# Performance work log

Measured on AMD Instinct MI355X. Metric: run time of the kernel, lower is better.

Reference implementation:

```python
import jax, jax.numpy as jnp
import numpy as np

B, D, H, O, E, R, K, NH = 2048, 512, 2048, 512, 8, 4, 2, 8
DH = O // NH
EPS = 1e-5

def _ln(x, g, b):
    m = x.mean(-1, keepdims=True)
    v = ((x - m) ** 2).mean(-1, keepdims=True)
    return (x - m) / jnp.sqrt(v + EPS) * g + b

def setup_inputs():
    key = jax.random.key(0)
    ks = jax.random.split(key, 16)
    n = lambda k, shape, fan: jax.random.normal(k, shape, jnp.float32) * (fan ** -0.5)
    x = jax.random.normal(ks[0], (B, D), jnp.float32)
    regime = jax.random.randint(ks[1], (B,), 0, R)
    regime_features = jax.nn.one_hot(regime, R, dtype=jnp.float32)
    return dict(
        x=x, regime=regime, regime_features=regime_features,
        ew1=n(ks[2], (R, E, D, H), D), eb1=jnp.zeros((R, E, H)),
        lng=jnp.ones((R, E, H)), lnb=jnp.zeros((R, E, H)),
        ew2=n(ks[3], (R, E, H, O), H), eb2=jnp.zeros((R, E, O)),
        rw1=n(ks[4], (R, D + R, H), D + R), rb1=jnp.zeros((R, H)),
        rw2=n(ks[5], (R, H, E), H), rb2=jnp.zeros((R, E)),
        ipw=n(ks[6], (3 * O, O), O), ipb=jnp.zeros((3 * O,)),
        opw=n(ks[7], (O, O), O), opb=jnp.zeros((O,)),
        ang=jnp.ones((O,)), anb=jnp.zeros((O,)),
    )

def _forward(x, regime, regime_features, ew1, eb1, lng, lnb, ew2, eb2, rw1, rb1, rw2, rb2, ipw, ipb, opw, opb, ang, anb):
    B_ = x.shape[0]
    bi = jnp.arange(B_)
    # regime-conditioned routing: compute logits for all regimes densely, select per sample
    ri = jnp.concatenate([x, regime_features], axis=-1)                  # [B, D+R]
    rh = jax.nn.relu(jnp.einsum('bf,rfh->rbh', ri, rw1) + rb1[:, None])
    logits = (jnp.einsum('rbh,rhe->rbe', rh, rw2) + rb2[:, None])[regime, bi]  # [B, E]
    w = jax.nn.softmax(logits, axis=-1)
    tkw, tki = jax.lax.top_k(w, K)
    tkw = tkw / tkw.sum(-1, keepdims=True)
    # experts: all regimes x all experts, then select the per-sample regime block
    h = jnp.einsum('bd,redh->rebh', x, ew1) + eb1[:, :, None]            # [R, E, B, H]
    h = jax.nn.relu(_ln(h, lng[:, :, None], lnb[:, :, None]))
    eo = jnp.einsum('rebh,reho->rebo', h, ew2) + eb2[:, :, None] + x[None, None]  # identity residual (D == O)
    eo = eo.transpose(0, 2, 1, 3)[regime, bi]                            # [B, E, O]
    # group attention over expert axis (torch MultiheadAttention, eval mode)
    qkv = eo @ ipw.T + ipb
    q, k, v = jnp.split(qkv, 3, axis=-1)
    sh = lambda t: t.reshape(B_, E, NH, DH).transpose(0, 2, 1, 3)
    q, k, v = sh(q), sh(k), sh(v)
    attn = jax.nn.softmax(jnp.einsum('bhqd,bhkd->bhqk', q, k) / np.sqrt(DH).astype(np.float32), axis=-1)
    av = jnp.einsum('bhqk,bhkd->bhqd', attn, v).transpose(0, 2, 1, 3).reshape(B_, E, O)
    eo = _ln(eo + av @ opw.T + opb, ang, anb)
    # top-k combine
    gathered = jnp.take_along_axis(eo, tki[:, :, None], axis=1)          # [B, K, O]
    return jnp.sum(tkw[:, :, None] * gathered, axis=1)

def reference(x, regime, regime_features, ew1, eb1, lng, lnb, ew2, eb2, rw1, rb1, rw2, rb2, ipw, ipb, opw, opb, ang, anb):
    return _forward(x, regime, regime_features, ew1, eb1, lng, lnb, ew2, eb2, rw1, rb1, rw2, rb2, ipw, ipb, opw, opb, ang, anb)
```

## Files before the change

### kernel.cpp

```cpp
#include <hip/hip_runtime.h>
#include <hip/hip_bf16.h>
#include <cstddef>

typedef __attribute__((ext_vector_type(8))) short short8;
typedef __attribute__((ext_vector_type(4))) float f32x4;

constexpr int CB = 2048;
constexpr int CD = 512;
constexpr int CH = 2048;
constexpr int CO = 512;
constexpr int CE = 8;
constexpr int CR = 4;
constexpr int MBY = 5;

__device__ __forceinline__ float bs2f(short s){
  union { float f; unsigned u; } u; u.u = ((unsigned)(unsigned short)s) << 16; return u.f;
}
__device__ __forceinline__ short f2bs(float x){
  union { __hip_bfloat16 h; short s; } u; u.h = __float2bfloat16(x); return u.s;
}

#define GLL(g, l) __builtin_amdgcn_global_load_lds((const __attribute__((address_space(1))) void*)(g), (__attribute__((address_space(3))) void*)(l), 16, 0, 0)

__device__ __forceinline__ short8 ln8(short8 raw, float mean, float rstd,
                                      float4 g01, float4 g23, float4 b01, float4 b23){
  const float g[8] = {g01.x,g01.y,g01.z,g01.w,g23.x,g23.y,g23.z,g23.w};
  const float b[8] = {b01.x,b01.y,b01.z,b01.w,b23.x,b23.y,b23.z,b23.w};
  short8 o;
#pragma unroll
  for (int j = 0; j < 8; j++){
    const float v = (bs2f(raw[j]) - mean) * rstd * g[j] + b[j];
    o[j] = f2bs(fmaxf(v, 0.f));
  }
  return o;
}

__device__ __forceinline__ void block_reduce2(float& a, float& b){
#pragma unroll
  for (int off = 32; off; off >>= 1){ a += __shfl_xor(a, off, 64); b += __shfl_xor(b, off, 64); }
  __shared__ float sa[4], sb[4];
  const int wid = threadIdx.x >> 6, lane = threadIdx.x & 63;
  __syncthreads();
  if (lane == 0){ sa[wid] = a; sb[wid] = b; }
  __syncthreads();
  a = sa[0] + sa[1] + sa[2] + sa[3];
  b = sb[0] + sb[1] + sb[2] + sb[3];
}

__global__ __launch_bounds__(1024) void k_bucket(const int* __restrict__ regime,
                                                 int* __restrict__ meta, int* __restrict__ perm){
  __shared__ int cnt[4], cur[4];
  const int t = threadIdx.x;
  if (t < 4) cnt[t] = 0;
  __syncthreads();
  const int r0 = regime[t];
  const int r1 = regime[t + 1024];
  atomicAdd(&cnt[r0], 1);
  atomicAdd(&cnt[r1], 1);
  __syncthreads();
  if (t == 0){
    const int c0 = cnt[0], c1 = cnt[1], c2 = cnt[2], c3 = cnt[3];
    meta[0] = 0; meta[1] = c0; meta[2] = c0 + c1; meta[3] = c0 + c1 + c2; meta[4] = c0 + c1 + c2 + c3;
    cur[0] = 0; cur[1] = c0; cur[2] = c0 + c1; cur[3] = c0 + c1 + c2;
  }
  __syncthreads();
  { int p = atomicAdd(&cur[r0], 1); perm[p] = t; }
  { int p = atomicAdd(&cur[r1], 1); perm[p] = t + 1024; }
}

__device__ __forceinline__ void cvtt_tile(float (*tile)[65], const float* __restrict__ in,
                                          short* __restrict__ outp, int K, int N,
                                          int bx, int by, int bz){
  const int k0 = by * 64, n0 = bx * 64;
  const float* src = in + (size_t)bz * K * N;
  short* dst = outp + (size_t)bz * K * N;
  const int t = threadIdx.x;
  const int kk = t >> 4, nq = (t & 15) * 4;
#pragma unroll
  for (int j = 0; j < 4; j++){
    float4 v = *(const float4*)(src + (size_t)(k0 + kk + j * 16) * N + n0 + nq);
    tile[kk + j * 16][nq] = v.x; tile[kk + j * 16][nq + 1] = v.y;
    tile[kk + j * 16][nq + 2] = v.z; tile[kk + j * 16][nq + 3] = v.w;
  }
  __syncthreads();
  const int n = t >> 2, kq = (t & 3) * 16;
  short8 o0, o1;
#pragma unroll
  for (int j = 0; j < 8; j++) o0[j] = f2bs(tile[kq + j][n]);
#pragma unroll
  for (int j = 0; j < 8; j++) o1[j] = f2bs(tile[kq + 8 + j][n]);
  short* drow = dst + (size_t)(n0 + n) * K + k0 + kq;
  *(short8*)(drow) = o0;
  *(short8*)(drow + 8) = o1;
}

__global__ __launch_bounds__(256) void k_prep(
    const float* __restrict__ x, const int* __restrict__ perm,
    short* __restrict__ xp, short* __restrict__ xd,
    const float* __restrict__ rw1, const float* __restrict__ rb1,
    short* __restrict__ wtR, float* __restrict__ rbias,
    const float* __restrict__ ew1, short* __restrict__ wt1){
  __shared__ float tile[64][65];
  const int s = blockIdx.x;
  const int t = threadIdx.x;
  if (s < 2048){
    const int i = s, b = perm[i], c = t * 2;
    float2 v = *(const float2*)(x + (size_t)b * CD + c);
    short2 hi; hi.x = f2bs(v.x); hi.y = f2bs(v.y);
    short2 lo; lo.x = f2bs(v.x - bs2f(hi.x)); lo.y = f2bs(v.y - bs2f(hi.y));
    *(short2*)(xp + (size_t)i * CD + c) = hi;
    short* row = xd + (size_t)i * 1536;
    *(short2*)(row + c) = hi;
    *(short2*)(row + 512 + c) = hi;
    *(short2*)(row + 1024 + c) = lo;
    return;
  }
  if (s < 3072){
    const int i = s - 2048;
    const int bx = i & 31, by = (i >> 5) & 7, r = i >> 8;
    const int k0 = by * 64, n0 = bx * 64;
    const float* src = rw1 + (size_t)r * (CD + CR) * CH;
    short* dst = wtR + (size_t)r * CH * 1536;
    if (by == 0 && t < 64){
      const int n = n0 + t;
      rbias[r * CH + n] = rb1[(size_t)r * CH + n] + src[((size_t)(CD + r)) * CH + n];
    }
    const int kk = t >> 4, nq = (t & 15) * 4;
#pragma unroll
    for (int j = 0; j < 4; j++){
      float4 v = *(const float4*)(src + (size_t)(k0 + kk + j * 16) * CH + n0 + nq);
      tile[kk + j * 16][nq] = v.x; tile[kk + j * 16][nq + 1] = v.y;
      tile[kk + j * 16][nq + 2] = v.z; tile[kk + j * 16][nq + 3] = v.w;
    }
    __syncthreads();
    const int n = t >> 2, kq = (t & 3) * 16;
    short8 h0, h1, l0, l1;
#pragma unroll
    for (int j = 0; j < 8; j++){
      float f = tile[kq + j][n];
      short h = f2bs(f); h0[j] = h; l0[j] = f2bs(f - bs2f(h));
    }
#pragma unroll
    for (int j = 0; j < 8; j++){
      float f = tile[kq + 8 + j][n];
      short h = f2bs(f); h1[j] = h; l1[j] = f2bs(f - bs2f(h));
    }
    short* drow = dst + (size_t)(n0 + n) * 1536;
    *(short8*)(drow + k0 + kq) = h0;        *(short8*)(drow + k0 + kq + 8) = h1;
    *(short8*)(drow + 512 + k0 + kq) = l0;  *(short8*)(drow + 512 + k0 + kq + 8) = l1;
    *(short8*)(drow + 1024 + k0 + kq) = h0; *(short8*)(drow + 1024 + k0 + kq + 8) = h1;
    return;
  }
  {
    const int i = s - 3072;
    cvtt_tile(tile, ew1, wt1, CD, CH, i & 31, (i >> 5) & 7, i >> 8);
  }
}

__device__ __forceinline__ void logits_body(int blk,
    const float* __restrict__ part, const float* __restrict__ rb2,
    const int* __restrict__ meta, const int* __restrict__ perm,
    int* __restrict__ tki, float* __restrict__ tkw, int* __restrict__ qrows){
  const int wid = threadIdx.x >> 6, lane = threadIdx.x & 63;
  const int i = blk * 4 + wid;
  const int r = (i >= meta[1]) + (i >= meta[2]) + (i >= meta[3]);
  const int p0 = lane >> 3, e = lane & 7;
  float v = 0.f;
#pragma unroll
  for (int j = 0; j < 4; j++)
    v += part[((size_t)(p0 + 8 * j) * CB + i) * 8 + e];
  v += __shfl_xor(v, 8, 64);
  v += __shfl_xor(v, 16, 64);
  v += __shfl_xor(v, 32, 64);
  v += rb2[r * CE + e];
  float l8[8];
#pragma unroll
  for (int e2 = 0; e2 < 8; e2++) l8[e2] = __shfl(v, e2, 64);
  if (lane == 0){
    int i1 = 0; float m1 = l8[0];
#pragma unroll
    for (int e2 = 1; e2 < 8; e2++) if (l8[e2] > m1){ m1 = l8[e2]; i1 = e2; }
    int i2 = -1; float m2 = -1e30f;
#pragma unroll
    for (int e2 = 0; e2 < 8; e2++) if (e2 != i1 && l8[e2] > m2){ m2 = l8[e2]; i2 = e2; }
    const float e2w = __expf(m2 - m1);
    const float w1 = 1.f / (1.f + e2w);
    const int b = perm[i];
    tki[b * 2] = i1; tki[b * 2 + 1] = i2;
    tkw[b * 2] = w1; tkw[b * 2 + 1] = e2w * w1;
    qrows[b * 2] = b * CE + i1; qrows[b * 2 + 1] = b * CE + i2;
  }
}

template<int EPI, int NB>
__device__ __forceinline__ void gemm_body(
    short* __restrict__ ldsb,
    int bx, int by, int bz,
    const short* __restrict__ A, long lda,
    const short* __restrict__ Wt, long ldw,
    const int* __restrict__ goff, int fixedM, int Ksub, int N,
    const float* __restrict__ bias, long bstride,
    short* __restrict__ outb, float* __restrict__ outf,
    const int* __restrict__ operm, const float* __restrict__ xtra,
    float* __restrict__ pstat){
  constexpr int BK = 32;
  constexpr int BSTR = 4096 + NB * 1024;

  const int z = bz;
  int g0 = 0, Mg = fixedM;
  if (goff){ const int r = (EPI == 6) ? z : (z >> 3); g0 = goff[r]; Mg = goff[r + 1] - g0; }
  const int m0 = by * 128;
  if (m0 >= Mg) return;
  const int n0 = bx * (NB * 32);
  const int e = z & 7;

  const short* Ab;
  if constexpr (EPI == 1 || EPI == 6) Ab = A + (size_t)g0 * (size_t)lda;
  else Ab = A;
  const short* Wb = Wt + (size_t)z * (size_t)N * (size_t)ldw;

  const int tid = threadIdx.x;
  const int lane = tid & 63, wid = tid >> 6;
  const int srow = lane >> 2;
  const int sc = (((lane & 3) ^ ((srow >> 1) & 3)) << 3);

  int ar0 = m0 + wid * 32 + srow;
  int ar1 = ar0 + 16;
  if (ar0 > Mg - 1) ar0 = Mg - 1;
  if (ar1 > Mg - 1) ar1 = Mg - 1;
  if constexpr (EPI == 3){
    if (operm){ ar0 = operm[ar0]; ar1 = operm[ar1]; }
  }
  const short* ga0 = Ab + (size_t)ar0 * lda + sc;
  const short* ga1 = Ab + (size_t)ar1 * lda + sc;
  const int brow = n0 + wid * (NB * 8) + srow;
  const short* gb0 = Wb + (size_t)brow * ldw + sc;
  const short* gb1 = gb0 + (size_t)16 * ldw;

  const int wm = (wid >> 1) * 64, wn = (wid & 1) * (NB * 16);
  const int r16 = lane & 15, kb = lane >> 4;
  const int rsw = (r16 >> 1) & 3;

  f32x4 acc[4][NB];
#pragma unroll
  for (int a = 0; a < 4; a++)
#pragma unroll
    for (int b = 0; b < NB; b++) acc[a][b] = (f32x4){0.f, 0.f, 0.f, 0.f};

  const int NT = Ksub / BK;
  int buf = 0;

  {
    short* dA = ldsb + wid * 1024;
    short* dB = ldsb + 4096 + wid * (NB * 256);
    GLL(ga0, dA); GLL(ga1, dA + 512);
    GLL(gb0, dB);
    if constexpr (NB == 4){ GLL(gb1, dB + 512); }
  }
  __syncthreads();

  for (int t = 0; t < NT; ++t){
    if (t + 1 < NT){
      const int kof = (t + 1) * BK;
      short* dA = ldsb + (buf ^ 1) * BSTR + wid * 1024;
      short* dB = ldsb + (buf ^ 1) * BSTR + 4096 + wid * (NB * 256);
      GLL(ga0 + kof, dA); GLL(ga1 + kof, dA + 512);
      GLL(gb0 + kof, dB);
      if constexpr (NB == 4){ GLL(gb1 + kof, dB + 512); }
    }
    const short* sA = ldsb + buf * BSTR;
    const short* sB = sA + 4096;
    short8 af[4], bfv[NB];
#pragma unroll
    for (int mi = 0; mi < 4; mi++)
      af[mi] = *(const short8*)(sA + (wm + mi * 16 + r16) * 32 + ((kb ^ rsw) << 3));
#pragma unroll
    for (int ni = 0; ni < NB; ni++)
      bfv[ni] = *(const short8*)(sB + (wn + ni * 16 + r16) * 32 + ((kb ^ rsw) << 3));
#pragma unroll
    for (int mi = 0; mi < 4; mi++)
#pragma unroll
      for (int ni = 0; ni < NB; ni++)
        acc[mi][ni] = __builtin_amdgcn_mfma_f32_16x16x32_bf16(af[mi], bfv[ni], acc[mi][ni], 0, 0, 0);
    __syncthreads();
    buf ^= 1;
  }

  if constexpr (EPI == 1){
    const int slot = bx * 2 + (wid & 1);
#pragma unroll
    for (int mi = 0; mi < 4; mi++){
#pragma unroll
      for (int q = 0; q < 4; q++){
        const int i = m0 + wm + mi * 16 + kb * 4 + q;
        float vv[NB]; float sv = 0.f, sq = 0.f;
#pragma unroll
        for (int ni = 0; ni < NB; ni++){
          const int n = n0 + wn + ni * 16 + r16;
          const float v = acc[mi][ni][q] + bias[(size_t)z * bstride + n];
          vv[ni] = v; sv += v; sq += v * v;
        }
#pragma unroll
        for (int off = 1; off < 16; off <<= 1){
          sv += __shfl_xor(sv, off, 64);
          sq += __shfl_xor(sq, off, 64);
        }
        if (i < Mg){
#pragma unroll
          for (int ni = 0; ni < NB; ni++){
            const int n = n0 + wn + ni * 16 + r16;
            outb[((size_t)e * CB + (g0 + i)) * (size_t)N + n] = f2bs(vv[ni]);
          }
          if (r16 == 0){
            float* sp = pstat + ((size_t)slot * (CE * CB) + (size_t)e * CB + (g0 + i)) * 2;
            sp[0] = sv; sp[1] = sq;
          }
        }
      }
    }
    return;
  }

  if constexpr (EPI == 6){
    const int hbase = n0 + wn;
    float wv[NB][8]; float rbv[NB];
#pragma unroll
    for (int ni = 0; ni < NB; ni++){
      const int h = hbase + ni * 16 + r16;
      rbv[ni] = bias[(size_t)z * CH + h];
      const float* wp = xtra + ((size_t)z * CH + h) * 8;
#pragma unroll
      for (int e2 = 0; e2 < 8; e2++) wv[ni][e2] = wp[e2];
    }
    const int slot = bx * 2 + (wid & 1);
#pragma unroll
    for (int mi = 0; mi < 4; mi++){
#pragma unroll
      for (int q = 0; q < 4; q++){
        float tmp[8];
#pragma unroll
        for (int e2 = 0; e2 < 8; e2++) tmp[e2] = 0.f;
#pragma unroll
        for (int ni = 0; ni < NB; ni++){
          const float v = fmaxf(acc[mi][ni][q] + rbv[ni], 0.f);
#pragma unroll
          for (int e2 = 0; e2 < 8; e2++) tmp[e2] += v * wv[ni][e2];
        }
#pragma unroll
        for (int e2 = 0; e2 < 8; e2++){
          tmp[e2] += __shfl_xor(tmp[e2], 1, 64);
          tmp[e2] += __shfl_xor(tmp[e2], 2, 64);
          tmp[e2] += __shfl_xor(tmp[e2], 4, 64);
          tmp[e2] += __shfl_xor(tmp[e2], 8, 64);
        }
        const int row = wm + mi * 16 + kb * 4 + q;
        if (r16 == 0 && m0 + row < Mg){
          float* dp = outf + ((size_t)slot * CB + (g0 + m0 + row)) * 8;
#pragma unroll
          for (int e2 = 0; e2 < 8; e2++) dp[e2] = tmp[e2];
        }
      }
    }
    return;
  }

#pragma unroll
  for (int mi = 0; mi < 4; mi++){
#pragma unroll
    for (int q = 0; q < 4; q++){
      const int i = m0 + wm + mi * 16 + kb * 4 + q;
      if (i >= Mg) continue;
#pragma unroll
      for (int ni = 0; ni < NB; ni++){
        const int n = n0 + wn + ni * 16 + r16;
        float v = acc[mi][ni][q] + bias[n];
        if constexpr (EPI == 3){
          outb[(size_t)i * (size_t)N + n] = f2bs(v);
        } else {
          outf[(size_t)i * (size_t)N + n] = v;
        }
      }
    }
  }
}

__global__ __launch_bounds__(256) void k_rg1(
    const short* __restrict__ xp, const short* __restrict__ wt1, const int* __restrict__ meta,
    const float* __restrict__ eb1, short* __restrict__ hact, float* __restrict__ pstat,
    const short* __restrict__ xd, const short* __restrict__ wtR,
    const float* __restrict__ rbias, const float* __restrict__ rw2, float* __restrict__ part,
    const float* __restrict__ ew2, short* __restrict__ wt2,
    const float* __restrict__ ipw, short* __restrict__ ipwb,
    const float* __restrict__ opw, short* __restrict__ opwb){
  __shared__ __align__(16) short lds[2][8192];
  const int s = blockIdx.x;
  if (s < 320){
    const int bx = s & 15, by = (s >> 4) % MBY, bz = s / (16 * MBY);
    gemm_body<6, 4>(&lds[0][0], bx, by, bz, xd, 1536, wtR, 1536, meta, 0, 1536, CH,
                    rbias, 0, nullptr, part, nullptr, rw2, nullptr);
  } else if (s < 2880){
    const int t = s - 320;
    const int l = (t & 7) * 320 + (t >> 3);
    const int bx = l % 16; const int u = l / 16; const int by = u % MBY; const int bz = u / MBY;
    gemm_body<1, 4>(&lds[0][0], bx, by, bz, xp, CD, wt1, CD, meta, 0, CD, CH, eb1, CH,
                    hact, nullptr, nullptr, nullptr, pstat);
  } else if (s < 11072){
    float (*tile)[65] = (float(*)[65])&lds[0][0];
    const int i = s - 2880;
    cvtt_tile(tile, ew2, wt2, CH, CO, i & 7, (i >> 3) & 31, i >> 8);
  } else {
    int i = ((s - 11072) * 256 + threadIdx.x) * 8;
    const int na = 1536 * 512, nb = 512 * 512;
    const float* src; short* dst;
    if (i < na){ src = ipw + i; dst = ipwb + i; }
    else { int j = i - na; if (j >= nb) return; src = opw + j; dst = opwb + j; }
    float4 u = *(const float4*)(src);
    float4 v = *(const float4*)(src + 4);
    short8 o;
    o[0]=f2bs(u.x); o[1]=f2bs(u.y); o[2]=f2bs(u.z); o[3]=f2bs(u.w);
    o[4]=f2bs(v.x); o[5]=f2bs(v.y); o[6]=f2bs(v.z); o[7]=f2bs(v.w);
    *(short8*)(dst) = o;
  }
}

__global__ __launch_bounds__(256) void k_g2l(
    const short* __restrict__ hact, const short* __restrict__ Wt,
    const int* __restrict__ goff, const float* __restrict__ pstat,
    const float* __restrict__ lng, const float* __restrict__ lnb,
    short* __restrict__ P, long pstr, const int* __restrict__ operm,
    const float* __restrict__ part, const float* __restrict__ rb2,
    int* __restrict__ tki, float* __restrict__ tkw, int* __restrict__ qrows){
  constexpr int BK = 32, KS = 1024;
  __shared__ __align__(16) short lds[2][8192];
  __shared__ float smean[128], srstd[128];

  const int s0 = blockIdx.x;
  if (s0 < 512){
    logits_body(s0, part, rb2, goff, operm, tki, tkw, qrows);
    return;
  }
  const int s = s0 - 512;
  const int l = (s & 7) * 160 + (s >> 3);
  const int bx = l % 4; const int u = l / 4; const int by = u % MBY; const int bz = u / MBY;
  const int ks = bz & 1, z = bz >> 1;
  const int r = z >> 3, e = z & 7;
  const int g0 = goff[r], Mg = goff[r + 1] - g0;
  const int m0 = by * 128;
  if (m0 >= Mg) return;
  const int n0 = bx * 128;
  const long kbase = (long)ks * KS;

  const int tid = threadIdx.x, lane = tid & 63, wid = tid >> 6;

  if (tid < 128){
    int lr = m0 + tid; if (lr > Mg - 1) lr = Mg - 1;
    const size_t rid = (size_t)e * CB + g0 + lr;
    float S = 0.f, Q = 0.f;
#pragma unroll
    for (int p = 0; p < 32; p++){
      const float2 pp = *(const float2*)(pstat + ((size_t)p * (CE * CB) + rid) * 2);
      S += pp.x; Q += pp.y;
    }
    const float mean = S * (1.f / CH);
    const float var = Q * (1.f / CH) - mean * mean;
    smean[tid] = mean;
    srstd[tid] = rsqrtf(fmaxf(var, 0.f) + 1e-5f);
  }

  const int srow = lane >> 2;
  const int c = lane & 3;
  const int dsw = (srow >> 1) & 3;

  const int lr0 = wid * 32 + srow, lr1 = lr0 + 16;
  const int cr0 = (m0 + lr0 > Mg - 1) ? (Mg - 1 - m0) : lr0;
  const int cr1 = (m0 + lr1 > Mg - 1) ? (Mg - 1 - m0) : lr1;

  const short* ga0 = hact + ((size_t)e * CB + g0 + (m0 + cr0)) * (size_t)CH + kbase + c * 8;
  const short* ga1 = hact + ((size_t)e * CB + g0 + (m0 + cr1)) * (size_t)CH + kbase + c * 8;
  const float* gp = lng + (size_t)(r * CE + e) * CH + kbase + c * 8;
  const float* bp = lnb + (size_t)(r * CE + e) * CH + kbase + c * 8;

  const short* Wb = Wt + (size_t)z * (size_t)CO * (size_t)CH;
  const int brow = n0 + wid * 32 + srow;
  const int scB = ((c ^ dsw) << 3);
  const short* gb0 = Wb + (size_t)brow * CH + kbase + scB;
  const short* gb1 = gb0 + (size_t)16 * CH;

  const int wof0 = lr0 * 32 + ((c ^ dsw) << 3);
  const int wof1 = lr1 * 32 + ((c ^ dsw) << 3);

  __syncthreads();
  const float mean0 = smean[cr0], rstd0 = srstd[cr0];
  const float mean1 = smean[cr1], rstd1 = srstd[cr1];

  const int wm = (wid >> 1) * 64, wn = (wid & 1) * 64;
  const int r16 = lane & 15, kb = lane >> 4;
  const int rsw = (r16 >> 1) & 3;

  f32x4 acc[4][4];
#pragma unroll
  for (int a = 0; a < 4; a++)
#pragma unroll
    for (int b = 0; b < 4; b++) acc[a][b] = (f32x4){0.f, 0.f, 0.f, 0.f};

  const int NT = KS / BK;
  int buf = 0;

  {
    short8 a0 = *(const short8*)(ga0);
    short8 a1 = *(const short8*)(ga1);
    float4 g01 = *(const float4*)(gp), g23 = *(const float4*)(gp + 4);
    float4 b01 = *(const float4*)(bp), b23 = *(const float4*)(bp + 4);
    short* dB = &lds[0][4096] + wid * 1024;
    GLL(gb0, dB); GLL(gb1, dB + 512);
    *(short8*)(&lds[0][0] + wof0) = ln8(a0, mean0, rstd0, g01, g23, b01, b23);
    *(short8*)(&lds[0][0] + wof1) = ln8(a1, mean1, rstd1, g01, g23, b01, b23);
  }
  __syncthreads();

  for (int t = 0; t < NT; ++t){
    short8 na0, na1; float4 ng01, ng23, nb01, nb23;
    if (t + 1 < NT){
      const int kof = (t + 1) * BK;
      na0 = *(const short8*)(ga0 + kof);
      na1 = *(const short8*)(ga1 + kof);
      ng01 = *(const float4*)(gp + kof); ng23 = *(const float4*)(gp + kof + 4);
      nb01 = *(const float4*)(bp + kof); nb23 = *(const float4*)(bp + kof + 4);
      short* dB = &lds[buf ^ 1][4096] + wid * 1024;
      GLL(gb0 + kof, dB); GLL(gb1 + kof, dB + 512);
    }
    const short* sA = &lds[buf][0];
    const short* sB = &lds[buf][4096];
    short8 af[4], bfv[4];
#pragma unroll
    for (int mi = 0; mi < 4; mi++)
      af[mi] = *(const short8*)(sA + (wm + mi * 16 + r16) * 32 + ((kb ^ rsw) << 3));
#pragma unroll
    for (int ni = 0; ni < 4; ni++)
      bfv[ni] = *(const short8*)(sB + (wn + ni * 16 + r16) * 32 + ((kb ^ rsw) << 3));
#pragma unroll
    for (int mi = 0; mi < 4; mi++)
#pragma unroll
      for (int ni = 0; ni < 4; ni++)
        acc[mi][ni] = __builtin_amdgcn_mfma_f32_16x16x32_bf16(af[mi], bfv[ni], acc[mi][ni], 0, 0, 0);
    if (t + 1 < NT){
      *(short8*)(&lds[buf ^ 1][0] + wof0) = ln8(na0, mean0, rstd0, ng01, ng23, nb01, nb23);
      *(short8*)(&lds[buf ^ 1][0] + wof1) = ln8(na1, mean1, rstd1, ng01, ng23, nb01, nb23);
    }
    __syncthreads();
    buf ^= 1;
  }

#pragma unroll
  for (int mi = 0; mi < 4; mi++){
#pragma unroll
    for (int q = 0; q < 4; q++){
      const int i = m0 + wm + mi * 16 + kb * 4 + q;
      if (i >= Mg) continue;
      const int borig = operm[g0 + i];
#pragma unroll
      for (int ni = 0; ni < 4; ni++){
        const int n = n0 + wn + ni * 16 + r16;
        P[(size_t)ks * pstr + ((size_t)borig * CE + e) * (size_t)CO + n] = f2bs(acc[mi][ni][q]);
      }
    }
  }
}

__global__ __launch_bounds__(256) void k_kvq(
    const short* __restrict__ eo, const short* __restrict__ ipwb, const float* __restrict__ ipb,
    short* __restrict__ qkv, short* __restrict__ qb, const int* __restrict__ qrows){
  __shared__ __align__(16) short lds[2][8192];
  const int s = blockIdx.x;
  if (s < 1024){
    const int chunk = 128;
    const int l = (s & 7) * chunk + (s >> 3);
    const int bx = l % 8, by = l / 8;
    gemm_body<3, 4>(&lds[0][0], bx, by, 0, eo, CO, ipwb + (size_t)512 * 512, CO, nullptr,
                    CB * CE, CO, 1024, ipb + 512, 0, qkv, nullptr, nullptr, nullptr, nullptr);
  } else {
    const int i = s - 1024;
    gemm_body<3, 4>(&lds[0][0], i & 3, i >> 2, 0, eo, CO, ipwb, CO, nullptr,
                    CB * 2, CO, CO, ipb, 0, qb, nullptr, qrows, nullptr, nullptr);
  }
}

__global__ __launch_bounds__(256) void k_proj(
    const short* __restrict__ av, const short* __restrict__ opwb, const float* __restrict__ opb,
    float* __restrict__ proj){
  __shared__ __align__(16) short lds[2][8192];
  gemm_body<4, 4>(&lds[0][0], blockIdx.x, blockIdx.y, 0, av, CO, opwb, CO, nullptr,
                  CB * 2, CO, CO, opb, 0, nullptr, proj, nullptr, nullptr, nullptr);
}

__global__ __launch_bounds__(256) void k_eo(const short* __restrict__ P, long pstr,
    const float* __restrict__ eb2, const float* __restrict__ x, const int* __restrict__ regime,
    short* __restrict__ eo){
  const int b = blockIdx.x, e = blockIdx.y;
  const int r = regime[b];
  const int c = threadIdx.x * 2;
  const size_t idx = (((size_t)b * CE + e) << 9) + c;
  short2 a0 = *(const short2*)(P + idx);
  short2 a1 = *(const short2*)(P + pstr + idx);
  float2 xr = *(const float2*)(x + (size_t)b * CD + c);
  float2 eb = *(const float2*)(eb2 + (((size_t)r * CE + e) << 9) + c);
  short2 o;
  o.x = f2bs(bs2f(a0.x) + bs2f(a1.x) + xr.x + eb.x);
  o.y = f2bs(bs2f(a0.y) + bs2f(a1.y) + xr.y + eb.y);
  *(short2*)(eo + idx) = o;
}

__global__ __launch_bounds__(128) void k_attn(const short* __restrict__ qb, const short* __restrict__ kv,
    const int* __restrict__ tki, short* __restrict__ av){
  const int b = blockIdx.x;
  const int j = threadIdx.x >> 6, d = threadIdx.x & 63;
  const short* q = qb + (size_t)(b * 2 + j) * CO;
  const short* base = kv + (size_t)b * CE * 1024;
#pragma unroll
  for (int h = 0; h < 8; h++){
    const float qv = bs2f(q[h * 64 + d]);
    float sc[8];
#pragma unroll
    for (int e = 0; e < 8; e++){
      float pp = qv * bs2f(base[(size_t)e * 1024 + h * 64 + d]);
#pragma unroll
      for (int off = 32; off; off >>= 1) pp += __shfl_xor(pp, off, 64);
      sc[e] = pp * 0.125f;
    }
    float m = sc[0];
#pragma unroll
    for (int e = 1; e < 8; e++) m = fmaxf(m, sc[e]);
    float den = 0.f, avd = 0.f;
#pragma unroll
    for (int e = 0; e < 8; e++){
      const float pe = __expf(sc[e] - m);
      den += pe;
      avd += pe * bs2f(base[(size_t)e * 1024 + 512 + h * 64 + d]);
    }
    av[((size_t)b * 2 + j) * CO + h * 64 + d] = f2bs(avd / den);
  }
}

__global__ __launch_bounds__(256) void k_final(const short* __restrict__ eo,
    const float* __restrict__ proj, const int* __restrict__ tki, const float* __restrict__ tkw,
    const float* __restrict__ ang, const float* __restrict__ anb, float* __restrict__ out){
  const int b = blockIdx.x, t = threadIdx.x;
  float o0 = 0.f, o1 = 0.f;
#pragma unroll
  for (int j = 0; j < 2; j++){
    const int s = tki[b * 2 + j];
    const float w = tkw[b * 2 + j];
    const short* ep = eo + ((size_t)b * CE + s) * CO;
    const float* pp = proj + ((size_t)b * 2 + j) * CO;
    const float v0 = bs2f(ep[t]) + pp[t];
    const float v1 = bs2f(ep[t + 256]) + pp[t + 256];
    float sm = v0 + v1, sq = v0 * v0 + v1 * v1;
    block_reduce2(sm, sq);
    const float mean = sm * (1.f / CO);
    const float rstd = rsqrtf(fmaxf(sq * (1.f / CO) - mean * mean, 0.f) + 1e-5f);
    o0 += w * ((v0 - mean) * rstd * ang[t] + anb[t]);
    o1 += w * ((v1 - mean) * rstd * ang[t + 256] + anb[t + 256]);
  }
  out[(size_t)b * CO + t] = o0;
  out[(size_t)b * CO + t + 256] = o1;
}

extern "C" void kernel_launch(void* const* d_in, const int* in_sizes, int n_in,
                              void* d_out, int out_size, void* d_ws, size_t ws_size,
                              hipStream_t stream){
  const float* x    = (const float*)d_in[0];
  const int*   regime = (const int*)d_in[1];
  const float* ew1  = (const float*)d_in[3];
  const float* eb1  = (const float*)d_in[4];
  const float* lng  = (const float*)d_in[5];
  const float* lnb  = (const float*)d_in[6];
  const float* ew2  = (const float*)d_in[7];
  const float* eb2  = (const float*)d_in[8];
  const float* rw1  = (const float*)d_in[9];
  const float* rb1  = (const float*)d_in[10];
  const float* rw2  = (const float*)d_in[11];
  const float* rb2  = (const float*)d_in[12];
  const float* ipw  = (const float*)d_in[13];
  const float* ipb  = (const float*)d_in[14];
  const float* opw  = (const float*)d_in[15];
  const float* opb  = (const float*)d_in[16];
  const float* ang  = (const float*)d_in[17];
  const float* anb  = (const float*)d_in[18];
  float* out = (float*)d_out;

  char* ws = (char*)d_ws;
  int*   meta  = (int*)(ws);
  int*   perm  = (int*)(ws + (16u << 10));
  int*   tki   = (int*)(ws + (32u << 10));
  float* tkw   = (float*)(ws + (48u << 10));
  int*   qrows = (int*)(ws + (64u << 10));
  float* rbias = (float*)(ws + (80u << 10));
  short* ipwb  = (short*)(ws + (256u << 10));
  short* opwb  = (short*)(ws + (1792u << 10));
  short* xp    = (short*)(ws + (2304u << 10));
  short* eo    = (short*)(ws + (4352u << 10));
  short* hact  = (short*)(ws + (22ull << 20));
  short* qkv   = (short*)(ws + (22ull << 20));
  short* qb    = (short*)(ws + (54ull << 20));
  short* av    = (short*)(ws + (58ull << 20));
  float* proj  = (float*)(ws + (62ull << 20));
  short* wtR   = (short*)(ws + (88ull << 20));
  short* wt1   = (short*)(ws + (112ull << 20));
  short* wt2   = (short*)(ws + (176ull << 20));
  short* P     = (short*)(ws + (240ull << 20));
  short* xd    = (short*)(ws + (272ull << 20));
  float* pstat = (float*)(ws + (280ull << 20));
  float* part  = (float*)(ws + (286ull << 20));
  const long PSTR = (long)CB * CE * CO;

  k_bucket<<<1, 1024, 0, stream>>>(regime, meta, perm);
  k_prep<<<11264, 256, 0, stream>>>(x, perm, xp, xd, rw1, rb1, wtR, rbias, ew1, wt1);
  k_rg1<<<320 + 2560 + 8192 + 512, 256, 0, stream>>>(
      xp, wt1, meta, eb1, hact, pstat, xd, wtR, rbias, rw2, part,
      ew2, wt2, ipw, ipwb, opw, opwb);
  k_g2l<<<512 + 1280, 256, 0, stream>>>(hact, wt2, meta, pstat, lng, lnb, P, PSTR, perm,
                                        part, rb2, tki, tkw, qrows);
  k_eo<<<dim3(CB, CE), 256, 0, stream>>>(P, PSTR, eb2, x, regime, eo);
  k_kvq<<<1024 + 128, 256, 0, stream>>>(eo, ipwb, ipb, qkv, qb, qrows);
  k_attn<<<CB, 128, 0, stream>>>(qb, qkv, tki, av);
  k_proj<<<dim3(4, 32), 256, 0, stream>>>(av, opwb, opb, proj);
  k_final<<<CB, 256, 0, stream>>>(eo, proj, tki, tkw, ang, anb, out);
  (void)in_sizes; (void)n_in; (void)out_size; (void)ws_size;
}
```

Baseline: 365.9 us.

## Drop split-K in second expert GEMM and fuse bias+residual epilogue

The second expert GEMM drops its two-way split-K and uses narrower 128x64 tiles across the full K range, keeping the same block count. This lets the epilogue add eb2 and the x residual and write bf16 eo directly. The separate k_eo reduction kernel and the partial-sum buffer P go away, which removes a launch and a large write-then-read round trip. In exchange each block runs twice as many K iterations with less MFMA work per A-tile load, so A-operand traffic and the LayerNorm recompute double.

```diff
diff --git a/kernel.cpp b/kernel.cpp
--- a/kernel.cpp
+++ b/kernel.cpp
@@ -427,11 +427,13 @@
     const short* __restrict__ hact, const short* __restrict__ Wt,
     const int* __restrict__ goff, const float* __restrict__ pstat,
     const float* __restrict__ lng, const float* __restrict__ lnb,
-    short* __restrict__ P, long pstr, const int* __restrict__ operm,
+    short* __restrict__ eo, const float* __restrict__ eb2, const float* __restrict__ xf,
+    const int* __restrict__ operm,
     const float* __restrict__ part, const float* __restrict__ rb2,
     int* __restrict__ tki, float* __restrict__ tkw, int* __restrict__ qrows){
-  constexpr int BK = 32, KS = 1024;
-  __shared__ __align__(16) short lds[2][8192];
+  constexpr int BK = 32, KS = 2048;
+  constexpr int BSTR = 6144;
+  __shared__ __align__(16) short lds[2][6144];
   __shared__ float smean[128], srstd[128];
 
   const int s0 = blockIdx.x;
@@ -441,14 +443,13 @@
   }
   const int s = s0 - 512;
   const int l = (s & 7) * 160 + (s >> 3);
-  const int bx = l % 4; const int u = l / 4; const int by = u % MBY; const int bz = u / MBY;
-  const int ks = bz & 1, z = bz >> 1;
+  const int bx = l % 8; const int u = l / 8; const int by = u % MBY; const int bz = u / MBY;
+  const int z = bz;
   const int r = z >> 3, e = z & 7;
   const int g0 = goff[r], Mg = goff[r + 1] - g0;
   const int m0 = by * 128;
   if (m0 >= Mg) return;
-  const int n0 = bx * 128;
-  const long kbase = (long)ks * KS;
+  const int n0 = bx * 64;
 
   const int tid = threadIdx.x, lane = tid & 63, wid = tid >> 6;
 
@@ -475,16 +476,15 @@
   const int cr0 = (m0 + lr0 > Mg - 1) ? (Mg - 1 - m0) : lr0;
   const int cr1 = (m0 + lr1 > Mg - 1) ? (Mg - 1 - m0) : lr1;
 
-  const short* ga0 = hact + ((size_t)e * CB + g0 + (m0 + cr0)) * (size_t)CH + kbase + c * 8;
-  const short* ga1 = hact + ((size_t)e * CB + g0 + (m0 + cr1)) * (size_t)CH + kbase + c * 8;
-  const float* gp = lng + (size_t)(r * CE + e) * CH + kbase + c * 8;
-  const float* bp = lnb + (size_t)(r * CE + e) * CH + kbase + c * 8;
+  const short* ga0 = hact + ((size_t)e * CB + g0 + (m0 + cr0)) * (size_t)CH + c * 8;
+  const short* ga1 = hact + ((size_t)e * CB + g0 + (m0 + cr1)) * (size_t)CH + c * 8;
+  const float* gp = lng + (size_t)(r * CE + e) * CH + c * 8;
+  const float* bp = lnb + (size_t)(r * CE + e) * CH + c * 8;
 
   const short* Wb = Wt + (size_t)z * (size_t)CO * (size_t)CH;
-  const int brow = n0 + wid * 32 + srow;
+  const int brow = n0 + wid * 16 + srow;
   const int scB = ((c ^ dsw) << 3);
-  const short* gb0 = Wb + (size_t)brow * CH + kbase + scB;
-  const short* gb1 = gb0 + (size_t)16 * CH;
+  const short* gb0 = Wb + (size_t)brow * CH + scB;
 
   const int wof0 = lr0 * 32 + ((c ^ dsw) << 3);
   const int wof1 = lr1 * 32 + ((c ^ dsw) << 3);
@@ -493,15 +493,15 @@
   const float mean0 = smean[cr0], rstd0 = srstd[cr0];
   const float mean1 = smean[cr1], rstd1 = srstd[cr1];
 
-  const int wm = (wid >> 1) * 64, wn = (wid & 1) * 64;
+  const int wm = (wid >> 1) * 64, wn = (wid & 1) * 32;
   const int r16 = lane & 15, kb = lane >> 4;
   const int rsw = (r16 >> 1) & 3;
 
-  f32x4 acc[4][4];
+  f32x4 acc[4][2];
 #pragma unroll
   for (int a = 0; a < 4; a++)
 #pragma unroll
-    for (int b = 0; b < 4; b++) acc[a][b] = (f32x4){0.f, 0.f, 0.f, 0.f};
+    for (int b = 0; b < 2; b++) acc[a][b] = (f32x4){0.f, 0.f, 0.f, 0.f};
 
   const int NT = KS / BK;
   int buf = 0;
@@ -511,8 +511,8 @@
     short8 a1 = *(const short8*)(ga1);
     float4 g01 = *(const float4*)(gp), g23 = *(const float4*)(gp + 4);
     float4 b01 = *(const float4*)(bp), b23 = *(const float4*)(bp + 4);
-    short* dB = &lds[0][4096] + wid * 1024;
-    GLL(gb0, dB); GLL(gb1, dB + 512);
+    short* dB = &lds[0][4096] + wid * 512;
+    GLL(gb0, dB);
     *(short8*)(&lds[0][0] + wof0) = ln8(a0, mean0, rstd0, g01, g23, b01, b23);
     *(short8*)(&lds[0][0] + wof1) = ln8(a1, mean1, rstd1, g01, g23, b01, b23);
   }
@@ -526,22 +526,22 @@
       na1 = *(const short8*)(ga1 + kof);
       ng01 = *(const float4*)(gp + kof); ng23 = *(const float4*)(gp + kof + 4);
       nb01 = *(const float4*)(bp + kof); nb23 = *(const float4*)(bp + kof + 4);
-      short* dB = &lds[buf ^ 1][4096] + wid * 1024;
-      GLL(gb0 + kof, dB); GLL(gb1 + kof, dB + 512);
+      short* dB = &lds[buf ^ 1][4096] + wid * 512;
+      GLL(gb0 + kof, dB);
     }
     const short* sA = &lds[buf][0];
-    const short* sB = &lds[buf][4096];
-    short8 af[4], bfv[4];
+    const short* sB = sA + 4096;
+    short8 af[4], bfv[2];
 #pragma unroll
     for (int mi = 0; mi < 4; mi++)
       af[mi] = *(const short8*)(sA + (wm + mi * 16 + r16) * 32 + ((kb ^ rsw) << 3));
 #pragma unroll
-    for (int ni = 0; ni < 4; ni++)
+    for (int ni = 0; ni < 2; ni++)
       bfv[ni] = *(const short8*)(sB + (wn + ni * 16 + r16) * 32 + ((kb ^ rsw) << 3));
 #pragma unroll
     for (int mi = 0; mi < 4; mi++)
 #pragma unroll
-      for (int ni = 0; ni < 4; ni++)
+      for (int ni = 0; ni < 2; ni++)
         acc[mi][ni] = __builtin_amdgcn_mfma_f32_16x16x32_bf16(af[mi], bfv[ni], acc[mi][ni], 0, 0, 0);
     if (t + 1 < NT){
       *(short8*)(&lds[buf ^ 1][0] + wof0) = ln8(na0, mean0, rstd0, ng01, ng23, nb01, nb23);
@@ -559,9 +559,11 @@
       if (i >= Mg) continue;
       const int borig = operm[g0 + i];
 #pragma unroll
-      for (int ni = 0; ni < 4; ni++){
+      for (int ni = 0; ni < 2; ni++){
         const int n = n0 + wn + ni * 16 + r16;
-        P[(size_t)ks * pstr + ((size_t)borig * CE + e) * (size_t)CO + n] = f2bs(acc[mi][ni][q]);
+        const float v = acc[mi][ni][q] + eb2[((size_t)r * CE + e) * CO + n]
+                      + xf[(size_t)borig * CD + n];
+        eo[((size_t)borig * CE + e) * (size_t)CO + n] = f2bs(v);
       }
     }
   }
@@ -591,23 +593,6 @@
   __shared__ __align__(16) short lds[2][8192];
   gemm_body<4, 4>(&lds[0][0], blockIdx.x, blockIdx.y, 0, av, CO, opwb, CO, nullptr,
                   CB * 2, CO, CO, opb, 0, nullptr, proj, nullptr, nullptr, nullptr);
-}
-
-__global__ __launch_bounds__(256) void k_eo(const short* __restrict__ P, long pstr,
-    const float* __restrict__ eb2, const float* __restrict__ x, const int* __restrict__ regime,
-    short* __restrict__ eo){
-  const int b = blockIdx.x, e = blockIdx.y;
-  const int r = regime[b];
-  const int c = threadIdx.x * 2;
-  const size_t idx = (((size_t)b * CE + e) << 9) + c;
-  short2 a0 = *(const short2*)(P + idx);
-  short2 a1 = *(const short2*)(P + pstr + idx);
-  float2 xr = *(const float2*)(x + (size_t)b * CD + c);
-  float2 eb = *(const float2*)(eb2 + (((size_t)r * CE + e) << 9) + c);
-  short2 o;
-  o.x = f2bs(bs2f(a0.x) + bs2f(a1.x) + xr.x + eb.x);
-  o.y = f2bs(bs2f(a0.y) + bs2f(a1.y) + xr.y + eb.y);
-  *(short2*)(eo + idx) = o;
 }
 
 __global__ __launch_bounds__(128) void k_attn(const short* __restrict__ qb, const short* __restrict__ kv,
@@ -707,20 +692,18 @@
   short* wtR   = (short*)(ws + (88ull << 20));
   short* wt1   = (short*)(ws + (112ull << 20));
   short* wt2   = (short*)(ws + (176ull << 20));
-  short* P     = (short*)(ws + (240ull << 20));
   short* xd    = (short*)(ws + (272ull << 20));
   float* pstat = (float*)(ws + (280ull << 20));
   float* part  = (float*)(ws + (286ull << 20));
-  const long PSTR = (long)CB * CE * CO;
 
   k_bucket<<<1, 1024, 0, stream>>>(regime, meta, perm);
   k_prep<<<11264, 256, 0, stream>>>(x, perm, xp, xd, rw1, rb1, wtR, rbias, ew1, wt1);
   k_rg1<<<320 + 2560 + 8192 + 512, 256, 0, stream>>>(
       xp, wt1, meta, eb1, hact, pstat, xd, wtR, rbias, rw2, part,
       ew2, wt2, ipw, ipwb, opw, opwb);
-  k_g2l<<<512 + 1280, 256, 0, stream>>>(hact, wt2, meta, pstat, lng, lnb, P, PSTR, perm,
+  k_g2l<<<512 + 1280, 256, 0, stream>>>(hact, wt2, meta, pstat, lng, lnb,
+                                        eo, eb2, x, perm,
                                         part, rb2, tki, tkw, qrows);
-  k_eo<<<dim3(CB, CE), 256, 0, stream>>>(P, PSTR, eb2, x, regime, eo);
   k_kvq<<<1024 + 128, 256, 0, stream>>>(eo, ipwb, ipb, qkv, qb, qrows);
   k_attn<<<CB, 128, 0, stream>>>(qb, qkv, tki, av);
   k_proj<<<dim3(4, 32), 256, 0, stream>>>(av, opwb, opb, proj);
```

New measurement: 401.4 us. 9.7% more time.
